# Kernel tuning notes

Measured on AMD Instinct MI355X. Metric: run time of the kernel, lower is better.

## Reference

```python
import jax, jax.numpy as jnp
import numpy as np
from jax import lax

N = 100000   # nodes
E = 3200000  # edges
D = 10       # feature dim (input_dim == output_dim == 10)
H = 16       # hidden dim of gnn1


def setup_inputs() -> dict:
    key = jax.random.key(0)
    ks = jax.random.split(key, 12)
    def g(k, shape, scale=0.1):
        return jax.random.normal(k, shape, jnp.float32) * scale
    return {
        "x": jax.random.normal(ks[0], (N, D), jnp.float32),
        "edge_index": jax.random.randint(ks[1], (2, E), 0, N, dtype=jnp.int32),
        "W1": g(ks[2], (D, H)),   # gnn1 weight
        "b1": jnp.zeros((H,), jnp.float32),
        "W2": g(ks[3], (H, D)),   # gnn2 weight
        "b2": jnp.zeros((D,), jnp.float32),
        "cW1": g(ks[4], (16, 1, 3)),   # Conv1d(1,16,3) OIH
        "cb1": jnp.zeros((16,), jnp.float32),
        "cW2": g(ks[5], (32, 16, 3)),  # Conv1d(16,32,3) OIH
        "cb2": jnp.zeros((32,), jnp.float32),
        "Wout": g(ks[6], (64, 2)),     # Linear(64, 2)
        "bout": jnp.zeros((2,), jnp.float32),
    }


def gcn_conv(x, src, dst, W, b, n):
    h = x @ W                                       # [N, F_out]
    loop = jnp.arange(n, dtype=src.dtype)
    s = jnp.concatenate([src, loop])
    d = jnp.concatenate([dst, loop])
    deg = jax.ops.segment_sum(jnp.ones(s.shape, h.dtype), d, num_segments=n)
    dinv = lax.rsqrt(jnp.maximum(deg, 1e-12))
    norm = dinv[s] * dinv[d]                        # [E+N]
    msg = h[s] * norm[:, None]                      # gather + scale
    out = jax.ops.segment_sum(msg, d, num_segments=n)  # scatter-add
    return out + b


def conv_block(x, W, b):
    # Conv1d(k=3, stride=1, pad=1) + ReLU + MaxPool1d(2)
    y = lax.conv_general_dilated(x, W, (1,), [(1, 1)],
                                 dimension_numbers=("NCH", "OIH", "NCH"))
    y = jax.nn.relu(y + b[None, :, None])
    return lax.reduce_window(y, -jnp.inf, lax.max, (1, 1, 2), (1, 1, 2), "VALID")


def reference(x, edge_index, W1, b1, W2, b2, cW1, cb1, cW2, cb2, Wout, bout):
    src, dst = edge_index[0], edge_index[1]
    n = x.shape[0]
    x_g = jax.nn.relu(gcn_conv(x, src, dst, W1, b1, n))
    # F.dropout with training=False is identity (eval mode)
    x_g = gcn_conv(x_g, src, dst, W2, b2, n)
    x_dual = x + x_g                                # residual add
    y = x_dual[:, None, :]                          # [N, 1, 10]
    y = conv_block(y, cW1, cb1)                     # [N, 16, 5]
    y = conv_block(y, cW2, cb2)                     # [N, 32, 2]
    y = y.reshape(n, -1)                            # [N, 64]
    out = y @ Wout + bout                           # [N, 2]
    return jax.nn.softmax(out, axis=1)
```

## Files before the change

### kernel.cpp

```cpp
#include <hip/hip_runtime.h>
#include <hip/hip_fp16.h>
#include <math.h>

#define TPB 256
#define TPB_C 512
#define NB_E 512
#define NPB 256
#define NBKT_CAP 512
#define BKT_STRIDE 8960
#define CHUNK_CAP 6272
#define GA_NODES 32

__global__ __launch_bounds__(TPB_C) void placeP_kernel(const int* __restrict__ ei, int E, int chunk, int nbkt,
                              int* __restrict__ gcur, unsigned* __restrict__ pairs) {
    __shared__ unsigned stg[CHUNK_CAP];
    __shared__ int lh[NBKT_CAP];
    __shared__ int lsc[NBKT_CAP];
    __shared__ int lcur[NBKT_CAP];
    __shared__ int gbase[NBKT_CAP];
    int blk = blockIdx.x;
    int t = threadIdx.x;
    lh[t] = 0;
    __syncthreads();
    int beg = blk * chunk;
    int end = beg + chunk; if (end > E) end = E;
    for (int k = beg + t; k < end; k += TPB_C)
        atomicAdd(&lh[ei[E + k] >> 8], 1);
    __syncthreads();
    int h = lh[t];
    lsc[t] = h;
    __syncthreads();
    for (int off = 1; off < NBKT_CAP; off <<= 1) {
        int v = (t >= off) ? lsc[t - off] : 0;
        __syncthreads();
        lsc[t] += v;
        __syncthreads();
    }
    lcur[t] = lsc[t] - h;
    if (t < nbkt && h > 0) gbase[t] = atomicAdd(&gcur[t], h);
    __syncthreads();
    for (int k = beg + t; k < end; k += TPB_C) {
        int s = ei[k];
        int d = ei[E + k];
        int pos = atomicAdd(&lcur[d >> 8], 1);
        stg[pos] = ((unsigned)s << 8) | (unsigned)(d & 255);
    }
    __syncthreads();
    int grp = t >> 4, lane = t & 15;
    for (int b = grp; b < nbkt; b += TPB_C / 16) {
        int len = lh[b];
        if (len == 0) continue;
        int ls = lsc[b] - len;
        int gb = gbase[b];
        int cap = BKT_STRIDE - gb;
        if (len > cap) len = (cap > 0) ? cap : 0;
        unsigned* dst = pairs + (size_t)b * BKT_STRIDE + gb;
        for (int i = lane; i < len; i += 16)
            dst[i] = stg[ls + i];
    }
}

__global__ __launch_bounds__(TPB) void sortD_kernel(unsigned* __restrict__ pairs,
                                                    const int* __restrict__ gcur, int N,
                                                    int2* __restrict__ rowbd,
                                                    float* __restrict__ dinv,
                                                    const float* __restrict__ x,
                                                    const float* __restrict__ W1,
                                                    __half* __restrict__ g1h) {
    __shared__ unsigned sp[BKT_STRIDE];
    __shared__ int lh[NPB];
    __shared__ int lsc[NPB];
    __shared__ int lcur[NPB];
    __shared__ float sW1[160];
    int b = blockIdx.x;
    size_t rbase = (size_t)b * BKT_STRIDE;
    int cnt = gcur[b];
    if (cnt > BKT_STRIDE) cnt = BKT_STRIDE;
    if (threadIdx.x < 160) sW1[threadIdx.x] = W1[threadIdx.x];
    for (int k = threadIdx.x; k < cnt; k += TPB) sp[k] = pairs[rbase + k];
    lh[threadIdx.x] = 0;
    __syncthreads();
    for (int k = threadIdx.x; k < cnt; k += TPB) atomicAdd(&lh[sp[k] & 255], 1);
    __syncthreads();
    int myh = lh[threadIdx.x];
    lsc[threadIdx.x] = myh;
    __syncthreads();
    for (int off = 1; off < NPB; off <<= 1) {
        int v = (threadIdx.x >= off) ? lsc[threadIdx.x - off] : 0;
        __syncthreads();
        lsc[threadIdx.x] += v;
        __syncthreads();
    }
    int excl = lsc[threadIdx.x] - myh;
    lcur[threadIdx.x] = excl;
    int v = b * NPB + threadIdx.x;
    float dv = rsqrtf((float)myh + 1.0f);
    if (v < N) {
        rowbd[v] = make_int2((int)(rbase + excl), myh);
        dinv[v] = dv;
    }
    __syncthreads();
    for (int k = threadIdx.x; k < cnt; k += TPB) {
        unsigned p = sp[k];
        int pos = atomicAdd(&lcur[p & 255], 1);
        pairs[rbase + pos] = p >> 8;
    }
    if (v < N) {
        float xv[10];
#pragma unroll
        for (int i = 0; i < 10; ++i) xv[i] = x[(size_t)v * 10 + i];
        float o[16];
#pragma unroll
        for (int j = 0; j < 16; ++j) {
            float hh = 0.f;
#pragma unroll
            for (int i = 0; i < 10; ++i) hh = fmaf(xv[i], sW1[i * 16 + j], hh);
            o[j] = hh * dv;
        }
        unsigned u[8];
#pragma unroll
        for (int q = 0; q < 8; ++q) {
            __half2 hh = __floats2half2_rn(o[2 * q], o[2 * q + 1]);
            u[q] = *reinterpret_cast<unsigned*>(&hh);
        }
        uint4* gp = (uint4*)(g1h + (size_t)v * 16);
        gp[0] = make_uint4(u[0], u[1], u[2], u[3]);
        gp[1] = make_uint4(u[4], u[5], u[6], u[7]);
    }
}

__device__ __forceinline__ void acc8(uint4 q, float* a) {
    __half2 h0 = *reinterpret_cast<__half2*>(&q.x);
    __half2 h1 = *reinterpret_cast<__half2*>(&q.y);
    __half2 h2 = *reinterpret_cast<__half2*>(&q.z);
    __half2 h3 = *reinterpret_cast<__half2*>(&q.w);
    float2 f0 = __half22float2(h0), f1 = __half22float2(h1);
    float2 f2 = __half22float2(h2), f3 = __half22float2(h3);
    a[0] += f0.x; a[1] += f0.y; a[2] += f1.x; a[3] += f1.y;
    a[4] += f2.x; a[5] += f2.y; a[6] += f3.x; a[7] += f3.y;
}

__device__ __forceinline__ void gather_core(int beg, int end, const unsigned* srcs,
                                            const uint4* gq, int pair, int half, float* a) {
#pragma unroll
    for (int i = 0; i < 8; ++i) a[i] = 0.f;
    int k = beg + pair;
    for (; k + 4 < end; k += 8) {
        unsigned s0 = srcs[k];
        unsigned s1 = srcs[k + 4];
        uint4 q0 = gq[(size_t)s0 * 2 + half];
        uint4 q1 = gq[(size_t)s1 * 2 + half];
        acc8(q0, a);
        acc8(q1, a);
    }
    if (k < end) acc8(gq[(size_t)srcs[k] * 2 + half], a);
#pragma unroll
    for (int i = 0; i < 8; ++i) a[i] += __shfl_xor(a[i], 2);
#pragma unroll
    for (int i = 0; i < 8; ++i) a[i] += __shfl_xor(a[i], 4);
}

__global__ __launch_bounds__(TPB) void gatherA_kernel(const int2* __restrict__ rowbd, const unsigned* __restrict__ srcs,
                               const uint4* __restrict__ g1q, const float* __restrict__ dinv,
                               const float* __restrict__ b1, const float* __restrict__ W2,
                               __half* __restrict__ g2h, int N) {
    __shared__ float sxg[GA_NODES][17];
    __shared__ float sdinv[GA_NODES];
    __shared__ float sW2[160];
    __shared__ float sb1[16];
    if (threadIdx.x < 160) sW2[threadIdx.x] = W2[threadIdx.x];
    if (threadIdx.x < 16) sb1[threadIdx.x] = b1[threadIdx.x];
    int grp = threadIdx.x >> 3;
    int lane8 = threadIdx.x & 7;
    int pair = lane8 >> 1, half = lane8 & 1;
    int v = blockIdx.x * GA_NODES + grp;
    float a[8];
    if (v < N) {
        int2 bd = rowbd[v];
        gather_core(bd.x, bd.x + bd.y, srcs, g1q, pair, half, a);
        if (lane8 < 2) {
            acc8(g1q[(size_t)v * 2 + half], a);
            float dv = dinv[v];
#pragma unroll
            for (int i = 0; i < 8; ++i)
                sxg[grp][half * 8 + i] = fmaxf(fmaf(dv, a[i], sb1[half * 8 + i]), 0.f);
            if (half == 0) sdinv[grp] = dv;
        }
    }
    __syncthreads();
    for (int idx = threadIdx.x; idx < GA_NODES * 16; idx += TPB) {
        int l2 = idx >> 4, i = idx & 15;
        int v2 = blockIdx.x * GA_NODES + l2;
        if (v2 < N) {
            float val = 0.f;
            if (i < 10) {
                float acc = 0.f;
#pragma unroll
                for (int jj = 0; jj < 16; ++jj) acc = fmaf(sxg[l2][jj], sW2[jj * 10 + i], acc);
                val = acc * sdinv[l2];
            }
            g2h[(size_t)v2 * 16 + i] = __float2half(val);
        }
    }
}

__global__ __launch_bounds__(TPB) void gatherB_kernel(const int2* __restrict__ rowbd, const unsigned* __restrict__ srcs,
                               const uint4* __restrict__ g2q, float* __restrict__ acc2, int N) {
    int grp = threadIdx.x >> 3;
    int lane8 = threadIdx.x & 7;
    int pair = lane8 >> 1, half = lane8 & 1;
    int v = blockIdx.x * GA_NODES + grp;
    if (v >= N) return;
    float a[8];
    int2 bd = rowbd[v];
    gather_core(bd.x, bd.x + bd.y, srcs, g2q, pair, half, a);
    if (lane8 < 2) {
        acc8(g2q[(size_t)v * 2 + half], a);
        float4* op = (float4*)(acc2 + (size_t)v * 16 + half * 8);
        op[0] = make_float4(a[0], a[1], a[2], a[3]);
        op[1] = make_float4(a[4], a[5], a[6], a[7]);
    }
}

__global__ void final_kernel(const float* __restrict__ x, const float* __restrict__ acc2,
                             const float* __restrict__ dinv, const float* __restrict__ b2,
                             const float* __restrict__ cW1, const float* __restrict__ cb1,
                             const float* __restrict__ cW2, const float* __restrict__ cb2,
                             const float* __restrict__ Wout, const float* __restrict__ bout,
                             float* __restrict__ out, int N) {
    __shared__ float s_cW1[48];
    __shared__ float s_cb1[16];
    __shared__ float s_cW2[1536];
    __shared__ float s_cb2[32];
    __shared__ float s_Wout[128];
    __shared__ float s_bout[2];
    for (int i = threadIdx.x; i < 48; i += blockDim.x) s_cW1[i] = cW1[i];
    for (int i = threadIdx.x; i < 16; i += blockDim.x) s_cb1[i] = cb1[i];
    for (int i = threadIdx.x; i < 1536; i += blockDim.x) s_cW2[i] = cW2[i];
    for (int i = threadIdx.x; i < 32; i += blockDim.x) s_cb2[i] = cb2[i];
    for (int i = threadIdx.x; i < 128; i += blockDim.x) s_Wout[i] = Wout[i];
    if (threadIdx.x < 2) s_bout[threadIdx.x] = bout[threadIdx.x];
    __syncthreads();

    int v = blockIdx.x * blockDim.x + threadIdx.x;
    if (v >= N) return;
    float dv = dinv[v];

    float xd[12];
    xd[0] = 0.f;
    xd[11] = 0.f;
#pragma unroll
    for (int i = 0; i < 10; ++i)
        xd[i + 1] = x[(size_t)v * 10 + i] + fmaf(dv, acc2[(size_t)v * 16 + i], b2[i]);

    float p1[16][7];
#pragma unroll
    for (int c = 0; c < 16; ++c) {
        float w0 = s_cW1[c * 3 + 0], w1 = s_cW1[c * 3 + 1], w2 = s_cW1[c * 3 + 2];
        float bc = s_cb1[c];
        p1[c][0] = 0.f;
        p1[c][6] = 0.f;
#pragma unroll
        for (int jj = 0; jj < 5; ++jj) {
            float y0 = fmaxf(fmaf(w0, xd[2 * jj + 0], fmaf(w1, xd[2 * jj + 1], fmaf(w2, xd[2 * jj + 2], bc))), 0.f);
            float y1 = fmaxf(fmaf(w0, xd[2 * jj + 1], fmaf(w1, xd[2 * jj + 2], fmaf(w2, xd[2 * jj + 3], bc))), 0.f);
            p1[c][jj + 1] = fmaxf(y0, y1);
        }
    }

    float z0 = s_bout[0], z1 = s_bout[1];
#pragma unroll
    for (int o = 0; o < 32; ++o) {
        float y2[5];
#pragma unroll
        for (int i = 0; i < 5; ++i) y2[i] = s_cb2[o];
#pragma unroll
        for (int c = 0; c < 16; ++c) {
            float w0 = s_cW2[o * 48 + c * 3 + 0];
            float w1 = s_cW2[o * 48 + c * 3 + 1];
            float w2 = s_cW2[o * 48 + c * 3 + 2];
#pragma unroll
            for (int i = 0; i < 5; ++i)
                y2[i] = fmaf(w0, p1[c][i], fmaf(w1, p1[c][i + 1], fmaf(w2, p1[c][i + 2], y2[i])));
        }
        float p20 = fmaxf(fmaxf(y2[0], 0.f), fmaxf(y2[1], 0.f));
        float p21 = fmaxf(fmaxf(y2[2], 0.f), fmaxf(y2[3], 0.f));
        z0 = fmaf(p20, s_Wout[(o * 2 + 0) * 2 + 0], z0);
        z1 = fmaf(p20, s_Wout[(o * 2 + 0) * 2 + 1], z1);
        z0 = fmaf(p21, s_Wout[(o * 2 + 1) * 2 + 0], z0);
        z1 = fmaf(p21, s_Wout[(o * 2 + 1) * 2 + 1], z1);
    }

    float m = fmaxf(z0, z1);
    float e0 = expf(z0 - m), e1 = expf(z1 - m);
    float inv = 1.f / (e0 + e1);
    out[(size_t)v * 2 + 0] = e0 * inv;
    out[(size_t)v * 2 + 1] = e1 * inv;
}

extern "C" void kernel_launch(void* const* d_in, const int* in_sizes, int n_in,
                              void* d_out, int out_size, void* d_ws, size_t ws_size,
                              hipStream_t stream) {
    const float* x    = (const float*)d_in[0];
    const int*   ei   = (const int*)d_in[1];
    const float* W1   = (const float*)d_in[2];
    const float* b1   = (const float*)d_in[3];
    const float* W2   = (const float*)d_in[4];
    const float* b2   = (const float*)d_in[5];
    const float* cW1  = (const float*)d_in[6];
    const float* cb1  = (const float*)d_in[7];
    const float* cW2  = (const float*)d_in[8];
    const float* cb2  = (const float*)d_in[9];
    const float* Wout = (const float*)d_in[10];
    const float* bout = (const float*)d_in[11];
    float* out = (float*)d_out;

    int N = in_sizes[0] / 10;
    int E = in_sizes[1] / 2;
    int nbkt = (N + NPB - 1) / NPB;
    int chunk = (E + NB_E - 1) / NB_E;
    int nb = (N + TPB - 1) / TPB;

    char* p = (char*)d_ws;
    int*      gcur  = (int*)p;       p += sizeof(int) * NBKT_CAP;
    unsigned* pairs = (unsigned*)p;  p += sizeof(unsigned) * (size_t)NBKT_CAP * BKT_STRIDE;
    int2*     rowbd = (int2*)p;      p += sizeof(int2) * (size_t)N;
    float*    dinv  = (float*)p;     p += sizeof(float) * (size_t)N;
    __half*   g1h   = (__half*)p;    p += sizeof(__half) * (size_t)16 * N;
    __half*   g2h   = (__half*)p;    p += sizeof(__half) * (size_t)16 * N;
    float*    acc2  = (float*)p;     p += sizeof(float) * (size_t)16 * N;

    hipMemsetAsync(gcur, 0, sizeof(int) * NBKT_CAP, stream);
    placeP_kernel<<<NB_E, TPB_C, 0, stream>>>(ei, E, chunk, nbkt, gcur, pairs);
    sortD_kernel<<<nbkt, TPB, 0, stream>>>(pairs, gcur, N, rowbd, dinv, x, W1, g1h);

    int ga = (N + GA_NODES - 1) / GA_NODES;
    gatherA_kernel<<<ga, TPB, 0, stream>>>(rowbd, pairs, (const uint4*)g1h, dinv, b1, W2, g2h, N);
    gatherB_kernel<<<ga, TPB, 0, stream>>>(rowbd, pairs, (const uint4*)g2h, acc2, N);
    final_kernel<<<nb, TPB, 0, stream>>>(x, acc2, dinv, b2, cW1, cb1, cW2, cb2, Wout, bout, out, N);
}
```

Before: 131.1 us.

## Fuse second gather with conv head and cache edge indices in registers

Merges the second GCN aggregation kernel with the final conv/linear/softmax kernel. The per-node accumulator now stays in shared memory instead of a global acc2 buffer, and the conv work is split across the 8 lanes of each node group with a shuffle reduction. The edge-placement kernel also loads src/dst into registers once and reuses them in the scatter pass, instead of reading global memory twice. The fixed NITER_C unroll assumes the per-block chunk is at most 13*512 edges, and the fusion adds extra shared memory and barriers.

```diff
diff --git a/kernel.cpp b/kernel.cpp
--- a/kernel.cpp
+++ b/kernel.cpp
@@ -5,6 +5,7 @@
 #define TPB 256
 #define TPB_C 512
 #define NB_E 512
+#define NITER_C 13
 #define NPB 256
 #define NBKT_CAP 512
 #define BKT_STRIDE 8960
@@ -24,8 +25,17 @@
     __syncthreads();
     int beg = blk * chunk;
     int end = beg + chunk; if (end > E) end = E;
-    for (int k = beg + t; k < end; k += TPB_C)
-        atomicAdd(&lh[ei[E + k] >> 8], 1);
+    unsigned rs[NITER_C], rd[NITER_C];
+#pragma unroll
+    for (int i = 0; i < NITER_C; ++i) {
+        int k = beg + t + i * TPB_C;
+        bool ok = k < end;
+        int s = ok ? ei[k] : 0;
+        int d = ok ? ei[E + k] : 0;
+        rs[i] = (unsigned)s;
+        rd[i] = (unsigned)d;
+        if (ok) atomicAdd(&lh[d >> 8], 1);
+    }
     __syncthreads();
     int h = lh[t];
     lsc[t] = h;
@@ -39,11 +49,13 @@
     lcur[t] = lsc[t] - h;
     if (t < nbkt && h > 0) gbase[t] = atomicAdd(&gcur[t], h);
     __syncthreads();
-    for (int k = beg + t; k < end; k += TPB_C) {
-        int s = ei[k];
-        int d = ei[E + k];
-        int pos = atomicAdd(&lcur[d >> 8], 1);
-        stg[pos] = ((unsigned)s << 8) | (unsigned)(d & 255);
+#pragma unroll
+    for (int i = 0; i < NITER_C; ++i) {
+        int k = beg + t + i * TPB_C;
+        if (k < end) {
+            int pos = atomicAdd(&lcur[rd[i] >> 8], 1);
+            stg[pos] = (rs[i] << 8) | (rd[i] & 255u);
+        }
     }
     __syncthreads();
     int grp = t >> 4, lane = t & 15;
@@ -204,98 +216,106 @@
     }
 }
 
-__global__ __launch_bounds__(TPB) void gatherB_kernel(const int2* __restrict__ rowbd, const unsigned* __restrict__ srcs,
-                               const uint4* __restrict__ g2q, float* __restrict__ acc2, int N) {
-    int grp = threadIdx.x >> 3;
-    int lane8 = threadIdx.x & 7;
-    int pair = lane8 >> 1, half = lane8 & 1;
-    int v = blockIdx.x * GA_NODES + grp;
-    if (v >= N) return;
-    float a[8];
-    int2 bd = rowbd[v];
-    gather_core(bd.x, bd.x + bd.y, srcs, g2q, pair, half, a);
-    if (lane8 < 2) {
-        acc8(g2q[(size_t)v * 2 + half], a);
-        float4* op = (float4*)(acc2 + (size_t)v * 16 + half * 8);
-        op[0] = make_float4(a[0], a[1], a[2], a[3]);
-        op[1] = make_float4(a[4], a[5], a[6], a[7]);
-    }
-}
-
-__global__ void final_kernel(const float* __restrict__ x, const float* __restrict__ acc2,
-                             const float* __restrict__ dinv, const float* __restrict__ b2,
-                             const float* __restrict__ cW1, const float* __restrict__ cb1,
-                             const float* __restrict__ cW2, const float* __restrict__ cb2,
-                             const float* __restrict__ Wout, const float* __restrict__ bout,
-                             float* __restrict__ out, int N) {
+__global__ __launch_bounds__(TPB) void gatherBF_kernel(const int2* __restrict__ rowbd, const unsigned* __restrict__ srcs,
+                               const uint4* __restrict__ g2q, const float* __restrict__ x,
+                               const float* __restrict__ dinv, const float* __restrict__ b2,
+                               const float* __restrict__ cW1, const float* __restrict__ cb1,
+                               const float* __restrict__ cW2, const float* __restrict__ cb2,
+                               const float* __restrict__ Wout, const float* __restrict__ bout,
+                               float* __restrict__ out, int N) {
+    __shared__ float sacc[GA_NODES][17];
+    __shared__ float sdinv[GA_NODES];
+    __shared__ float sp1[GA_NODES][113];
     __shared__ float s_cW1[48];
     __shared__ float s_cb1[16];
     __shared__ float s_cW2[1536];
     __shared__ float s_cb2[32];
     __shared__ float s_Wout[128];
+    __shared__ float s_b2[10];
     __shared__ float s_bout[2];
-    for (int i = threadIdx.x; i < 48; i += blockDim.x) s_cW1[i] = cW1[i];
-    for (int i = threadIdx.x; i < 16; i += blockDim.x) s_cb1[i] = cb1[i];
-    for (int i = threadIdx.x; i < 1536; i += blockDim.x) s_cW2[i] = cW2[i];
-    for (int i = threadIdx.x; i < 32; i += blockDim.x) s_cb2[i] = cb2[i];
-    for (int i = threadIdx.x; i < 128; i += blockDim.x) s_Wout[i] = Wout[i];
+    for (int i = threadIdx.x; i < 1536; i += TPB) s_cW2[i] = cW2[i];
+    if (threadIdx.x < 48) s_cW1[threadIdx.x] = cW1[threadIdx.x];
+    if (threadIdx.x < 16) s_cb1[threadIdx.x] = cb1[threadIdx.x];
+    if (threadIdx.x < 32) s_cb2[threadIdx.x] = cb2[threadIdx.x];
+    if (threadIdx.x < 128) s_Wout[threadIdx.x] = Wout[threadIdx.x];
+    if (threadIdx.x < 10) s_b2[threadIdx.x] = b2[threadIdx.x];
     if (threadIdx.x < 2) s_bout[threadIdx.x] = bout[threadIdx.x];
-    __syncthreads();
-
-    int v = blockIdx.x * blockDim.x + threadIdx.x;
-    if (v >= N) return;
-    float dv = dinv[v];
-
-    float xd[12];
-    xd[0] = 0.f;
-    xd[11] = 0.f;
-#pragma unroll
-    for (int i = 0; i < 10; ++i)
-        xd[i + 1] = x[(size_t)v * 10 + i] + fmaf(dv, acc2[(size_t)v * 16 + i], b2[i]);
-
-    float p1[16][7];
-#pragma unroll
-    for (int c = 0; c < 16; ++c) {
-        float w0 = s_cW1[c * 3 + 0], w1 = s_cW1[c * 3 + 1], w2 = s_cW1[c * 3 + 2];
-        float bc = s_cb1[c];
-        p1[c][0] = 0.f;
-        p1[c][6] = 0.f;
-#pragma unroll
-        for (int jj = 0; jj < 5; ++jj) {
-            float y0 = fmaxf(fmaf(w0, xd[2 * jj + 0], fmaf(w1, xd[2 * jj + 1], fmaf(w2, xd[2 * jj + 2], bc))), 0.f);
-            float y1 = fmaxf(fmaf(w0, xd[2 * jj + 1], fmaf(w1, xd[2 * jj + 2], fmaf(w2, xd[2 * jj + 3], bc))), 0.f);
-            p1[c][jj + 1] = fmaxf(y0, y1);
-        }
-    }
-
-    float z0 = s_bout[0], z1 = s_bout[1];
-#pragma unroll
-    for (int o = 0; o < 32; ++o) {
-        float y2[5];
-#pragma unroll
-        for (int i = 0; i < 5; ++i) y2[i] = s_cb2[o];
-#pragma unroll
-        for (int c = 0; c < 16; ++c) {
-            float w0 = s_cW2[o * 48 + c * 3 + 0];
-            float w1 = s_cW2[o * 48 + c * 3 + 1];
-            float w2 = s_cW2[o * 48 + c * 3 + 2];
-#pragma unroll
-            for (int i = 0; i < 5; ++i)
-                y2[i] = fmaf(w0, p1[c][i], fmaf(w1, p1[c][i + 1], fmaf(w2, p1[c][i + 2], y2[i])));
-        }
-        float p20 = fmaxf(fmaxf(y2[0], 0.f), fmaxf(y2[1], 0.f));
-        float p21 = fmaxf(fmaxf(y2[2], 0.f), fmaxf(y2[3], 0.f));
-        z0 = fmaf(p20, s_Wout[(o * 2 + 0) * 2 + 0], z0);
-        z1 = fmaf(p20, s_Wout[(o * 2 + 0) * 2 + 1], z1);
-        z0 = fmaf(p21, s_Wout[(o * 2 + 1) * 2 + 0], z0);
-        z1 = fmaf(p21, s_Wout[(o * 2 + 1) * 2 + 1], z1);
-    }
-
-    float m = fmaxf(z0, z1);
-    float e0 = expf(z0 - m), e1 = expf(z1 - m);
-    float inv = 1.f / (e0 + e1);
-    out[(size_t)v * 2 + 0] = e0 * inv;
-    out[(size_t)v * 2 + 1] = e1 * inv;
+
+    int grp = threadIdx.x >> 3;
+    int lane8 = threadIdx.x & 7;
+    int pair = lane8 >> 1, half = lane8 & 1;
+    int v = blockIdx.x * GA_NODES + grp;
+    if (v < N) {
+        float a[8];
+        int2 bd = rowbd[v];
+        gather_core(bd.x, bd.x + bd.y, srcs, g2q, pair, half, a);
+        if (lane8 < 2) {
+            acc8(g2q[(size_t)v * 2 + half], a);
+#pragma unroll
+            for (int i = 0; i < 8; ++i) sacc[grp][half * 8 + i] = a[i];
+            if (half == 0) sdinv[grp] = dinv[v];
+        }
+    }
+    __syncthreads();
+    if (v < N) {
+        float dv = sdinv[grp];
+        float xd[12];
+        xd[0] = 0.f; xd[11] = 0.f;
+#pragma unroll
+        for (int i = 0; i < 10; ++i)
+            xd[i + 1] = x[(size_t)v * 10 + i] + fmaf(dv, sacc[grp][i], s_b2[i]);
+#pragma unroll
+        for (int q = 0; q < 2; ++q) {
+            int c = lane8 * 2 + q;
+            float w0 = s_cW1[c * 3 + 0], w1 = s_cW1[c * 3 + 1], w2 = s_cW1[c * 3 + 2];
+            float bc = s_cb1[c];
+            sp1[grp][c * 7 + 0] = 0.f;
+            sp1[grp][c * 7 + 6] = 0.f;
+#pragma unroll
+            for (int jj = 0; jj < 5; ++jj) {
+                float y0 = fmaxf(fmaf(w0, xd[2 * jj + 0], fmaf(w1, xd[2 * jj + 1], fmaf(w2, xd[2 * jj + 2], bc))), 0.f);
+                float y1 = fmaxf(fmaf(w0, xd[2 * jj + 1], fmaf(w1, xd[2 * jj + 2], fmaf(w2, xd[2 * jj + 3], bc))), 0.f);
+                sp1[grp][c * 7 + jj + 1] = fmaxf(y0, y1);
+            }
+        }
+    }
+    __syncthreads();
+    if (v < N) {
+        float z0 = 0.f, z1 = 0.f;
+#pragma unroll
+        for (int q = 0; q < 4; ++q) {
+            int o = lane8 * 4 + q;
+            float y2[5];
+#pragma unroll
+            for (int i = 0; i < 5; ++i) y2[i] = s_cb2[o];
+#pragma unroll
+            for (int c = 0; c < 16; ++c) {
+                float w0 = s_cW2[o * 48 + c * 3 + 0];
+                float w1 = s_cW2[o * 48 + c * 3 + 1];
+                float w2 = s_cW2[o * 48 + c * 3 + 2];
+#pragma unroll
+                for (int i = 0; i < 5; ++i)
+                    y2[i] = fmaf(w0, sp1[grp][c * 7 + i], fmaf(w1, sp1[grp][c * 7 + i + 1], fmaf(w2, sp1[grp][c * 7 + i + 2], y2[i])));
+            }
+            float p20 = fmaxf(fmaxf(y2[0], 0.f), fmaxf(y2[1], 0.f));
+            float p21 = fmaxf(fmaxf(y2[2], 0.f), fmaxf(y2[3], 0.f));
+            z0 = fmaf(p20, s_Wout[(o * 2 + 0) * 2 + 0], z0);
+            z1 = fmaf(p20, s_Wout[(o * 2 + 0) * 2 + 1], z1);
+            z0 = fmaf(p21, s_Wout[(o * 2 + 1) * 2 + 0], z0);
+            z1 = fmaf(p21, s_Wout[(o * 2 + 1) * 2 + 1], z1);
+        }
+        z0 += __shfl_xor(z0, 1); z1 += __shfl_xor(z1, 1);
+        z0 += __shfl_xor(z0, 2); z1 += __shfl_xor(z1, 2);
+        z0 += __shfl_xor(z0, 4); z1 += __shfl_xor(z1, 4);
+        if (lane8 == 0) {
+            z0 += s_bout[0];
+            z1 += s_bout[1];
+            float m = fmaxf(z0, z1);
+            float e0 = expf(z0 - m), e1 = expf(z1 - m);
+            float inv = 1.f / (e0 + e1);
+            ((float2*)out)[v] = make_float2(e0 * inv, e1 * inv);
+        }
+    }
 }
 
 extern "C" void kernel_launch(void* const* d_in, const int* in_sizes, int n_in,
@@ -319,7 +339,7 @@
     int E = in_sizes[1] / 2;
     int nbkt = (N + NPB - 1) / NPB;
     int chunk = (E + NB_E - 1) / NB_E;
-    int nb = (N + TPB - 1) / TPB;
+    (void)nbkt;
 
     char* p = (char*)d_ws;
     int*      gcur  = (int*)p;       p += sizeof(int) * NBKT_CAP;
@@ -328,7 +348,6 @@
     float*    dinv  = (float*)p;     p += sizeof(float) * (size_t)N;
     __half*   g1h   = (__half*)p;    p += sizeof(__half) * (size_t)16 * N;
     __half*   g2h   = (__half*)p;    p += sizeof(__half) * (size_t)16 * N;
-    float*    acc2  = (float*)p;     p += sizeof(float) * (size_t)16 * N;
 
     hipMemsetAsync(gcur, 0, sizeof(int) * NBKT_CAP, stream);
     placeP_kernel<<<NB_E, TPB_C, 0, stream>>>(ei, E, chunk, nbkt, gcur, pairs);
@@ -336,6 +355,6 @@
 
     int ga = (N + GA_NODES - 1) / GA_NODES;
     gatherA_kernel<<<ga, TPB, 0, stream>>>(rowbd, pairs, (const uint4*)g1h, dinv, b1, W2, g2h, N);
-    gatherB_kernel<<<ga, TPB, 0, stream>>>(rowbd, pairs, (const uint4*)g2h, acc2, N);
-    final_kernel<<<nb, TPB, 0, stream>>>(x, acc2, dinv, b2, cW1, cb1, cW2, cb2, Wout, bout, out, N);
-}
+    gatherBF_kernel<<<ga, TPB, 0, stream>>>(rowbd, pairs, (const uint4*)g2h, x, dinv, b2,
+                                            cW1, cb1, cW2, cb2, Wout, bout, out, N);
+}
```

Measured after the change: 141.8 us. 8.2% more time.
